# Kernel optimization log

Hardware: AMD Instinct MI355X
Metric: run time of the kernel (lower is better)

The kernel has to match this reference:

```python
import jax, jax.numpy as jnp
import numpy as np

B, L, E, H = 8, 1024, 512, 8
E2 = 2 * E
EPS = 1e-5


def _spectral_fc(x, w, fw, fb, n):
    # rfft along feature dim, multiply by rfft of learned filter w (1,n), irfft back, then Linear
    xf = jnp.fft.rfft(x, axis=2, norm='ortho')          # [B,L,n//2+1] complex
    wf = jnp.fft.rfft(w, axis=1, norm='ortho')          # [1,n//2+1] complex
    y = jnp.fft.irfft(xf * wf, n=n, axis=2, norm='ortho')
    return y @ fw + fb


def _layernorm(x, g, b):
    m = jnp.mean(x, axis=-1, keepdims=True)
    v = jnp.mean(jnp.square(x - m), axis=-1, keepdims=True)
    return (x - m) * jax.lax.rsqrt(v + EPS) * g + b


def setup_inputs() -> dict:
    key = jax.random.key(0)
    ks = jax.random.split(key, 32)
    s = 0.02

    def lin_w(k, i, o):
        return (jax.random.normal(k, (i, o), jnp.float32) / np.sqrt(i)).astype(jnp.float32)

    def layer_params(k0, k1, n):
        return (s * jax.random.normal(k0, (1, n), jnp.float32), lin_w(k1, n, n), jnp.zeros((n,), jnp.float32))

    attn_w, attn_fw, attn_fb = layer_params(ks[1], ks[2], E)
    ln0_w, ln0_fw, ln0_fb = layer_params(ks[3], ks[4], E)
    ln1_w, ln1_fw, ln1_fb = layer_params(ks[5], ks[6], E)
    ln2_w, ln2_fw, ln2_fb = layer_params(ks[7], ks[8], E)
    ln3_w, ln3_fw, ln3_fb = layer_params(ks[9], ks[10], E2)
    ln4_w, ln4_fw, ln4_fb = layer_params(ks[11], ks[12], E2)

    return {
        'x': jax.random.normal(ks[0], (B, L, E), jnp.float32),
        'attn_w': attn_w, 'attn_fw': attn_fw, 'attn_fb': attn_fb,
        'ln0_w': ln0_w, 'ln0_fw': ln0_fw, 'ln0_fb': ln0_fb,
        'ln1_w': ln1_w, 'ln1_fw': ln1_fw, 'ln1_fb': ln1_fb,
        'ln2_w': ln2_w, 'ln2_fw': ln2_fw, 'ln2_fb': ln2_fb,
        'ln3_w': ln3_w, 'ln3_fw': ln3_fw, 'ln3_fb': ln3_fb,
        'ln4_w': ln4_w, 'ln4_fw': ln4_fw, 'ln4_fb': ln4_fb,
        'n1_g': jnp.ones((E,), jnp.float32), 'n1_b': jnp.zeros((E,), jnp.float32),
        'n2_g': jnp.ones((E,), jnp.float32), 'n2_b': jnp.zeros((E,), jnp.float32),
    }


def reference(x, attn_w, attn_fw, attn_fb,
              ln0_w, ln0_fw, ln0_fb, ln1_w, ln1_fw, ln1_fb,
              ln2_w, ln2_fw, ln2_fb, ln3_w, ln3_fw, ln3_fb,
              ln4_w, ln4_fw, ln4_fb, n1_g, n1_b, n2_g, n2_b):
    q = _spectral_fc(x, attn_w, attn_fw, attn_fb, E).reshape(B, L, H, E // H)
    scores = jnp.einsum('blhe,bshe->bhls', q, q) * (1.0 / np.sqrt(E))
    A = jax.nn.softmax(scores, axis=-1)
    new_x = jnp.einsum('bhls,bshd->blhd', A, q).reshape(B, L, E)

    x1 = _layernorm(x + new_x, n1_g, n1_b)
    x_ln = jax.nn.gelu(_spectral_fc(x1, ln0_w, ln0_fw, ln0_fb, E), approximate=False)
    x2 = x1 - x_ln
    h = jax.nn.sigmoid(_spectral_fc(x2, ln1_w, ln1_fw, ln1_fb, E)) * _spectral_fc(x2, ln2_w, ln2_fw, ln2_fb, E)
    out = jnp.concatenate((new_x, x_ln), axis=-1)  # [B,L,2E]
    out = jax.nn.sigmoid(_spectral_fc(out, ln3_w, ln3_fw, ln3_fb, E2)) * _spectral_fc(out, ln4_w, ln4_fw, ln4_fb, E2)
    return (_layernorm(h, n2_g, n2_b), out)
```

## Files before the change

### kernel.cpp

```cpp
#include <hip/hip_runtime.h>
#include <hip/hip_bf16.h>
#include <math.h>

typedef __hip_bfloat16 bf16;
typedef unsigned short u16;
typedef __attribute__((ext_vector_type(8))) short short8;
typedef __attribute__((ext_vector_type(4))) float f32x4;

#define NB      8
#define SEQ     1024
#define EDIM    512
#define E2DIM   1024
#define ROWS    8192
#define INV_SQRT_E 0.04419417382415922f
#define ATT_SCL    0.06375985678148161f

__device__ inline u16 f2bu(float f) {
    union { float f; unsigned u; } c; c.f = f;
    return (u16)((c.u + 0x7FFF + ((c.u >> 16) & 1)) >> 16);
}

__device__ __forceinline__ unsigned cvtpk_bf16(float lo, float hi) {
    unsigned r;
    asm("v_cvt_pk_bf16_f32 %0, %1, %2" : "=v"(r) : "v"(lo), "v"(hi));
    return r;
}

#define VMCNT(N) do { \
    asm volatile("s_waitcnt vmcnt(" #N ")" ::: "memory"); \
    __builtin_amdgcn_sched_barrier(0); \
    __builtin_amdgcn_s_barrier(); \
    __builtin_amdgcn_sched_barrier(0); } while (0)

#define LGKM0_BAR() do { \
    asm volatile("s_waitcnt lgkmcnt(0)" ::: "memory"); \
    __builtin_amdgcn_sched_barrier(0); \
    __builtin_amdgcn_s_barrier(); \
    __builtin_amdgcn_sched_barrier(0); } while (0)

__global__ __launch_bounds__(256) void detect_dtype(const u16* __restrict__ x,
                                                    int* __restrict__ flag) {
    int t = threadIdx.x;
    int cnt = 0;
    for (int k = t; k < 8192; k += 256) {
        int e = (x[k] >> 7) & 0xFF;
        if (e >= 0xC0) cnt++;
    }
#pragma unroll
    for (int o = 32; o > 0; o >>= 1) cnt += __shfl_xor(cnt, o);
    __shared__ int red[4];
    if ((t & 63) == 0) red[t >> 6] = cnt;
    __syncthreads();
    if (t == 0) flag[0] = (red[0] + red[1] + red[2] + red[3] > 100) ? 1 : 0;
}

struct CvtBatch {
    const void* src[23];
    float4*     dst[23];
    int         pre4[24];
};

__global__ __launch_bounds__(256) void cvt_all(CvtBatch a, int total4,
                                               const int* __restrict__ flag) {
    int t = blockIdx.x * 256 + threadIdx.x;
    if (t >= total4) return;
    int lo = 0;
    while (t >= a.pre4[lo + 1]) lo++;
    int li = t - a.pre4[lo];
    if (flag[0]) {
        a.dst[lo][li] = ((const float4*)a.src[lo])[li];
    } else {
        ushort4 u = ((const ushort4*)a.src[lo])[li];
        union { unsigned int i; float f; } c;
        float4 o;
        c.i = ((unsigned)u.x) << 16; o.x = c.f;
        c.i = ((unsigned)u.y) << 16; o.y = c.f;
        c.i = ((unsigned)u.z) << 16; o.z = c.f;
        c.i = ((unsigned)u.w) << 16; o.w = c.f;
        a.dst[lo][li] = o;
    }
}

__global__ __launch_bounds__(256) void f2b_kernel(const float* __restrict__ src,
                                                  u16* __restrict__ dst, int n4) {
    int i = blockIdx.x * 256 + threadIdx.x;
    if (i >= n4) return;
    float4 a = ((const float4*)src)[i];
    ushort4 o;
    o.x = f2bu(a.x); o.y = f2bu(a.y); o.z = f2bu(a.z); o.w = f2bu(a.w);
    ((ushort4*)dst)[i] = o;
}

#define LDK 32

__device__ __forceinline__ void stage128x32(const u16* g, int ld, u16* lds, int tid) {
    const int w = tid >> 6;
    const int l = tid & 63;
    const int r = w * 16 + (l >> 2);
    const int c = ((l & 3) ^ ((l >> 3) & 3)) * 8;
    const u16* g0 = g + (size_t)r * ld + c;
    u16* l0 = lds + w * 16 * LDK;
    __builtin_amdgcn_global_load_lds(
        (const __attribute__((address_space(1))) void*)g0,
        (__attribute__((address_space(3))) void*)l0, 16, 0, 0);
    const u16* g1 = g0 + (size_t)64 * ld;
    u16* l1 = l0 + 64 * LDK;
    __builtin_amdgcn_global_load_lds(
        (const __attribute__((address_space(1))) void*)g1,
        (__attribute__((address_space(3))) void*)l1, 16, 0, 0);
}

__device__ __forceinline__ void stage64x32(const u16* g, int ld, u16* lds, int tid) {
    const int w = tid >> 6;
    const int l = tid & 63;
    const int r = w * 16 + (l >> 2);
    const int c = ((l & 3) ^ ((l >> 3) & 3)) * 8;
    const u16* g0 = g + (size_t)r * ld + c;
    u16* l0 = lds + w * 16 * LDK;
    __builtin_amdgcn_global_load_lds(
        (const __attribute__((address_space(1))) void*)g0,
        (__attribute__((address_space(3))) void*)l0, 16, 0, 0);
}

__device__ __forceinline__ void stage64x64sw(const u16* g0, int ld, u16* lds,
                                             int wave, int lane) {
#pragma unroll
    for (int c = 0; c < 2; c++) {
        const int r  = wave * 16 + c * 8 + (lane >> 3);
        const int cg = (lane & 7) ^ (r & 7);
        const u16* g = g0 + (size_t)r * ld + cg * 8;
        u16* l = lds + (wave * 16 + c * 8) * 64;
        __builtin_amdgcn_global_load_lds(
            (const __attribute__((address_space(1))) void*)g,
            (__attribute__((address_space(3))) void*)l, 16, 0, 0);
    }
}

__device__ __forceinline__ void xcd_swz(int& bx, int& by) {
    const int nx  = gridDim.x;
    const int nwg = nx * gridDim.y;
    const int lid = blockIdx.y * nx + blockIdx.x;
    const int q   = nwg >> 3;
    const int s   = (lid & 7) * q + (lid >> 3);
    bx = s % nx;
    by = s / nx;
}

struct FoldBatch {
    const float* w[6];
    const float* fw[6];
    u16* t1[6];
    u16* t2[6];
    u16* mt[6];
    int  n[6], lg[6];
    float sc[6];
};

__global__ __launch_bounds__(256) void fold_trconv(FoldBatch fb) {
    const int z = blockIdx.z;
    const int n = fb.n[z];
    const int bx = blockIdx.x * 32, by = blockIdx.y * 32;
    if (bx >= n || by >= n) return;
    __shared__ float t[32][33];
    const int tx = threadIdx.x & 31, ty = threadIdx.x >> 5;
    const float* src = fb.fw[z];
    u16* dst = fb.t1[z];
#pragma unroll
    for (int r = 0; r < 32; r += 8)
        t[ty + r][tx] = src[(size_t)(by + ty + r) * n + bx + tx];
    __syncthreads();
#pragma unroll
    for (int r = 0; r < 32; r += 8)
        dst[(size_t)(bx + ty + r) * n + by + tx] = f2bu(t[tx][ty + r]);
}

__global__ __launch_bounds__(256) void fold_circ(FoldBatch fb) {
    const int z = blockIdx.z;
    const int n = fb.n[z], lg = fb.lg[z];
    int idx = blockIdx.x * 256 + threadIdx.x;
    if (idx >= n * n) return;
    int mask = n - 1;
    int m = idx & mask;
    int j = idx >> lg;
    fb.t2[z][idx] = f2bu(fb.w[z][(m - j) & mask]);
}

__global__ __launch_bounds__(256) void fold_gemm(FoldBatch fb) {
    const int z = blockIdx.z;
    const int n = fb.n[z];
    const int bm = blockIdx.y * 128, bn = blockIdx.x * 128;
    if (bm >= n || bn >= n) return;
    const u16* A  = fb.t1[z];
    const u16* Bt = fb.t2[z];
    u16* Mt = fb.mt[z];
    const float scale = fb.sc[z];

    __shared__ u16 Asl[2][128 * LDK];
    __shared__ u16 Bsl[2][128 * LDK];
    const int tid = threadIdx.x;
    const int lane = tid & 63, wave = tid >> 6;
    const int wy = wave >> 1, wx = wave & 1;
    const int qd = lane >> 4, ln16 = lane & 15;
    const int ca = (qd ^ ((ln16 >> 1) & 3)) * 8;

    f32x4 acc[4][4];
#pragma unroll
    for (int i = 0; i < 4; i++)
#pragma unroll
        for (int j = 0; j < 4; j++)
#pragma unroll
            for (int r = 0; r < 4; r++) acc[i][j][r] = 0.f;

    const u16* Ab = A  + (size_t)bm * n;
    const u16* Bb = Bt + (size_t)bn * n;
    const int nt = n >> 5;
    stage128x32(Ab, n, Asl[0], tid);
    stage128x32(Bb, n, Bsl[0], tid);
    stage128x32(Ab + 32, n, Asl[1], tid);
    stage128x32(Bb + 32, n, Bsl[1], tid);
    int cur = 0;
    for (int t = 0; t < nt - 1; ++t) {
        VMCNT(4);
        const u16* Ac = Asl[cur];
        const u16* Bc = Bsl[cur];
        short8 af[4], bf_[4];
#pragma unroll
        for (int i = 0; i < 4; i++) {
            af[i]  = *(const short8*)&Ac[(wy * 64 + i * 16 + ln16) * LDK + ca];
            bf_[i] = *(const short8*)&Bc[(wx * 64 + i * 16 + ln16) * LDK + ca];
        }
        LGKM0_BAR();
        if (t + 2 < nt) {
            const int k2 = (t + 2) * 32;
            stage128x32(Ab + k2, n, Asl[cur], tid);
            stage128x32(Bb + k2, n, Bsl[cur], tid);
        }
#pragma unroll
        for (int i = 0; i < 4; i++)
#pragma unroll
            for (int j = 0; j < 4; j++)
                acc[i][j] = __builtin_amdgcn_mfma_f32_16x16x32_bf16(af[i], bf_[j], acc[i][j], 0, 0, 0);
        cur ^= 1;
    }
    VMCNT(0);
    {
        const u16* Ac = Asl[cur];
        const u16* Bc = Bsl[cur];
        short8 af[4], bf_[4];
#pragma unroll
        for (int i = 0; i < 4; i++) {
            af[i]  = *(const short8*)&Ac[(wy * 64 + i * 16 + ln16) * LDK + ca];
            bf_[i] = *(const short8*)&Bc[(wx * 64 + i * 16 + ln16) * LDK + ca];
        }
#pragma unroll
        for (int i = 0; i < 4; i++)
#pragma unroll
            for (int j = 0; j < 4; j++)
                acc[i][j] = __builtin_amdgcn_mfma_f32_16x16x32_bf16(af[i], bf_[j], acc[i][j], 0, 0, 0);
    }
#pragma unroll
    for (int i = 0; i < 4; i++)
#pragma unroll
        for (int j = 0; j < 4; j++) {
            const int col = bn + wx * 64 + j * 16 + ln16;
#pragma unroll
            for (int r = 0; r < 4; r++) {
                const int row = bm + wy * 64 + i * 16 + qd * 4 + r;
                Mt[(size_t)row * n + col] = f2bu(acc[i][j][r] * scale);
            }
        }
}

__global__ __launch_bounds__(256) void gemm_bf(
    const u16* __restrict__ A, int lda,
    const u16* __restrict__ Bt, int ldb,
    const float* __restrict__ bias,
    float* __restrict__ Cf, int ldc,
    u16* __restrict__ Cb, int ldcb,
    u16* __restrict__ Cb2, int ldcb2,
    const float* __restrict__ aux, int ldaux,
    int K, int mode)
{
    __shared__ u16 Asl[2][128 * LDK];
    __shared__ u16 Bsl[2][64 * LDK];
    const int tid = threadIdx.x;
    int bxs, bys;
    xcd_swz(bxs, bys);
    const int bm = bys * 128, bn = bxs * 64;
    const int lane = tid & 63, wave = tid >> 6;
    const int wy = wave >> 1, wx = wave & 1;
    const int qd = lane >> 4, ln16 = lane & 15;
    const int ca = (qd ^ ((ln16 >> 1) & 3)) * 8;

    f32x4 acc[4][2];
#pragma unroll
    for (int i = 0; i < 4; i++)
#pragma unroll
        for (int j = 0; j < 2; j++)
#pragma unroll
            for (int r = 0; r < 4; r++) acc[i][j][r] = 0.f;

    const u16* Ab = A  + (size_t)bm * lda;
    const u16* Bb = Bt + (size_t)bn * ldb;
    const int nt = K >> 5;
    stage128x32(Ab, lda, Asl[0], tid);
    stage64x32(Bb, ldb, Bsl[0], tid);
    stage128x32(Ab + 32, lda, Asl[1], tid);
    stage64x32(Bb + 32, ldb, Bsl[1], tid);
    int cur = 0;
    for (int t = 0; t < nt - 1; ++t) {
        VMCNT(3);
        const u16* Ac = Asl[cur];
        const u16* Bc = Bsl[cur];
        short8 af[4], bf_[2];
#pragma unroll
        for (int i = 0; i < 4; i++)
            af[i]  = *(const short8*)&Ac[(wy * 64 + i * 16 + ln16) * LDK + ca];
#pragma unroll
        for (int j = 0; j < 2; j++)
            bf_[j] = *(const short8*)&Bc[(wx * 32 + j * 16 + ln16) * LDK + ca];
        LGKM0_BAR();
        if (t + 2 < nt) {
            const int k2 = (t + 2) * 32;
            stage128x32(Ab + k2, lda, Asl[cur], tid);
            stage64x32(Bb + k2, ldb, Bsl[cur], tid);
        }
#pragma unroll
        for (int i = 0; i < 4; i++)
#pragma unroll
            for (int j = 0; j < 2; j++)
                acc[i][j] = __builtin_amdgcn_mfma_f32_16x16x32_bf16(af[i], bf_[j], acc[i][j], 0, 0, 0);
        cur ^= 1;
    }
    VMCNT(0);
    {
        const u16* Ac = Asl[cur];
        const u16* Bc = Bsl[cur];
        short8 af[4], bf_[2];
#pragma unroll
        for (int i = 0; i < 4; i++)
            af[i]  = *(const short8*)&Ac[(wy * 64 + i * 16 + ln16) * LDK + ca];
#pragma unroll
        for (int j = 0; j < 2; j++)
            bf_[j] = *(const short8*)&Bc[(wx * 32 + j * 16 + ln16) * LDK + ca];
#pragma unroll
        for (int i = 0; i < 4; i++)
#pragma unroll
            for (int j = 0; j < 2; j++)
                acc[i][j] = __builtin_amdgcn_mfma_f32_16x16x32_bf16(af[i], bf_[j], acc[i][j], 0, 0, 0);
    }

#pragma unroll
    for (int i = 0; i < 4; i++) {
#pragma unroll
        for (int j = 0; j < 2; j++) {
            const int col = bn + wx * 32 + j * 16 + ln16;
            const float b_ = bias ? bias[col] : 0.f;
#pragma unroll
            for (int r = 0; r < 4; r++) {
                const int row = bm + wy * 64 + i * 16 + qd * 4 + r;
                float v = acc[i][j][r] + b_;
                if (mode == 1) v = 0.5f * v * (1.0f + erff(v * 0.7071067811865476f));
                if (Cf)  Cf[(size_t)row * ldc + col] = v;
                if (Cb)  Cb[(size_t)row * ldcb + col] = f2bu(v);
                if (Cb2) Cb2[(size_t)row * ldcb2 + col] =
                             f2bu(aux[(size_t)row * ldaux + col] - v);
            }
        }
    }
}

__global__ __launch_bounds__(256) void gemm_bf2(
    const u16* __restrict__ A, int lda,
    const u16* __restrict__ B1t, const u16* __restrict__ B2t, int ldb,
    const float* __restrict__ bias1, const float* __restrict__ bias2,
    float* __restrict__ Cf, int ldc, int K)
{
    __shared__ u16 Asl[2][128 * LDK];
    __shared__ u16 B1sl[2][64 * LDK];
    __shared__ u16 B2sl[2][64 * LDK];
    const int tid = threadIdx.x;
    int bxs, bys;
    xcd_swz(bxs, bys);
    const int bm = bys * 128, bn = bxs * 64;
    const int lane = tid & 63, wave = tid >> 6;
    const int wy = wave >> 1, wx = wave & 1;
    const int qd = lane >> 4, ln16 = lane & 15;
    const int ca = (qd ^ ((ln16 >> 1) & 3)) * 8;

    f32x4 acc1[4][2], acc2[4][2];
#pragma unroll
    for (int i = 0; i < 4; i++)
#pragma unroll
        for (int j = 0; j < 2; j++)
#pragma unroll
            for (int r = 0; r < 4; r++) { acc1[i][j][r] = 0.f; acc2[i][j][r] = 0.f; }

    const u16* Ab  = A   + (size_t)bm * lda;
    const u16* B1b = B1t + (size_t)bn * ldb;
    const u16* B2b = B2t + (size_t)bn * ldb;
    const int nt = K >> 5;
    stage128x32(Ab,  lda, Asl[0],  tid);
    stage64x32(B1b, ldb, B1sl[0], tid);
    stage64x32(B2b, ldb, B2sl[0], tid);
    stage128x32(Ab + 32,  lda, Asl[1],  tid);
    stage64x32(B1b + 32, ldb, B1sl[1], tid);
    stage64x32(B2b + 32, ldb, B2sl[1], tid);
    int cur = 0;
    for (int t = 0; t < nt - 1; ++t) {
        VMCNT(4);
        const u16* Ac  = Asl[cur];
        const u16* B1c = B1sl[cur];
        const u16* B2c = B2sl[cur];
        short8 af[4], b1f[2], b2f[2];
#pragma unroll
        for (int i = 0; i < 4; i++)
            af[i]  = *(const short8*)&Ac [(wy * 64 + i * 16 + ln16) * LDK + ca];
#pragma unroll
        for (int j = 0; j < 2; j++) {
            b1f[j] = *(const short8*)&B1c[(wx * 32 + j * 16 + ln16) * LDK + ca];
            b2f[j] = *(const short8*)&B2c[(wx * 32 + j * 16 + ln16) * LDK + ca];
        }
        LGKM0_BAR();
        if (t + 2 < nt) {
            const int k2 = (t + 2) * 32;
            stage128x32(Ab  + k2, lda, Asl[cur],  tid);
            stage64x32(B1b + k2, ldb, B1sl[cur], tid);
            stage64x32(B2b + k2, ldb, B2sl[cur], tid);
        }
#pragma unroll
        for (int i = 0; i < 4; i++)
#pragma unroll
            for (int j = 0; j < 2; j++) {
                acc1[i][j] = __builtin_amdgcn_mfma_f32_16x16x32_bf16(af[i], b1f[j], acc1[i][j], 0, 0, 0);
                acc2[i][j] = __builtin_amdgcn_mfma_f32_16x16x32_bf16(af[i], b2f[j], acc2[i][j], 0, 0, 0);
            }
        cur ^= 1;
    }
    VMCNT(0);
    {
        const u16* Ac  = Asl[cur];
        const u16* B1c = B1sl[cur];
        const u16* B2c = B2sl[cur];
        short8 af[4], b1f[2], b2f[2];
#pragma unroll
        for (int i = 0; i < 4; i++)
            af[i]  = *(const short8*)&Ac [(wy * 64 + i * 16 + ln16) * LDK + ca];
#pragma unroll
        for (int j = 0; j < 2; j++) {
            b1f[j] = *(const short8*)&B1c[(wx * 32 + j * 16 + ln16) * LDK + ca];
            b2f[j] = *(const short8*)&B2c[(wx * 32 + j * 16 + ln16) * LDK + ca];
        }
#pragma unroll
        for (int i = 0; i < 4; i++)
#pragma unroll
            for (int j = 0; j < 2; j++) {
                acc1[i][j] = __builtin_amdgcn_mfma_f32_16x16x32_bf16(af[i], b1f[j], acc1[i][j], 0, 0, 0);
                acc2[i][j] = __builtin_amdgcn_mfma_f32_16x16x32_bf16(af[i], b2f[j], acc2[i][j], 0, 0, 0);
            }
    }

#pragma unroll
    for (int i = 0; i < 4; i++) {
#pragma unroll
        for (int j = 0; j < 2; j++) {
            const int col = bn + wx * 32 + j * 16 + ln16;
            const float b1_ = bias1[col], b2_ = bias2[col];
#pragma unroll
            for (int r = 0; r < 4; r++) {
                const int row = bm + wy * 64 + i * 16 + qd * 4 + r;
                const float g = 1.0f / (1.0f + expf(-(acc1[i][j][r] + b1_)));
                Cf[(size_t)row * ldc + col] = g * (acc2[i][j][r] + b2_);
            }
        }
    }
}

__global__ __launch_bounds__(256) void ln_kernel(
    const float* __restrict__ in0, int ld0,
    const u16* __restrict__ in1b, int ld1b,
    const float* __restrict__ g, const float* __restrict__ bta,
    float* __restrict__ outf, int ldo,
    u16* __restrict__ outb, int ldob)
{
    int row = blockIdx.x, tid = threadIdx.x;
    const float* p0 = in0 + (size_t)row * ld0;
    float v0 = p0[tid], v1 = p0[tid + 256];
    if (in1b) {
        const u16* p1 = in1b + (size_t)row * ld1b;
        union { unsigned u; float f; } c0, c1;
        c0.u = ((unsigned)p1[tid]) << 16;
        c1.u = ((unsigned)p1[tid + 256]) << 16;
        v0 += c0.f; v1 += c1.f;
    }
    float s = v0 + v1, sq = v0 * v0 + v1 * v1;
#pragma unroll
    for (int o = 32; o > 0; o >>= 1) {
        s  += __shfl_xor(s, o);
        sq += __shfl_xor(sq, o);
    }
    __shared__ float red[8];
    int wid = tid >> 6;
    if ((tid & 63) == 0) { red[wid] = s; red[4 + wid] = sq; }
    __syncthreads();
    s  = red[0] + red[1] + red[2] + red[3];
    sq = red[4] + red[5] + red[6] + red[7];
    float mean = s * (1.0f / 512.0f);
    float var  = sq * (1.0f / 512.0f) - mean * mean;
    float rstd = rsqrtf(var + 1e-5f);
    float o0 = (v0 - mean) * rstd * g[tid] + bta[tid];
    float o1 = (v1 - mean) * rstd * g[tid + 256] + bta[tid + 256];
    if (outf) {
        outf[(size_t)row * ldo + tid]       = o0;
        outf[(size_t)row * ldo + tid + 256] = o1;
    }
    if (outb) {
        outb[(size_t)row * ldob + tid]       = f2bu(o0);
        outb[(size_t)row * ldob + tid + 256] = f2bu(o1);
    }
}

__global__ __launch_bounds__(256) void trans_vt(const u16* __restrict__ q,
                                                u16* __restrict__ vt) {
    const int z  = blockIdx.z;
    const int bb = z >> 3, hh = z & 7;
    const int k0 = blockIdx.x * 64;
    const int d0 = blockIdx.y * 32;
    __shared__ u16 t[64][33];
    const int tx = threadIdx.x & 31, ty = threadIdx.x >> 5;
    const u16* src = q + (size_t)(bb * SEQ + k0) * EDIM + hh * 64 + d0;
#pragma unroll
    for (int r = 0; r < 64; r += 8)
        t[ty + r][tx] = src[(size_t)(ty + r) * EDIM + tx];
    __syncthreads();
    const int ox = threadIdx.x & 63, oy = threadIdx.x >> 6;
    u16* dst = vt + ((size_t)z * 64 + d0) * SEQ + k0;
#pragma unroll
    for (int r = 0; r < 32; r += 4)
        dst[(size_t)(oy + r) * SEQ + ox] = t[ox][oy + r];
}

#define AP 80
#define ANT 16

__global__ __launch_bounds__(256) void attn_mfma(const u16* __restrict__ qall,
                                                 const u16* __restrict__ vt,
                                                 u16* __restrict__ catb) {
    __shared__ u16 Ks[64 * 64];
    __shared__ u16 VTs[64 * 64];
    __shared__ u16 Pw[4][16 * AP];

    const int phys = blockIdx.x;
    const int bid = (phys & 7) * 128 + (phys >> 3);
    const int lt = bid & 15, hh = (bid >> 4) & 7, bb = bid >> 7;
    const int q0 = lt * 64;
    const int tid = threadIdx.x;
    const int wave = tid >> 6, lane = tid & 63;
    const int quad = lane >> 4, ln16 = lane & 15;

    const u16* qh = qall + (size_t)bb * SEQ * EDIM + hh * 64;
    const u16* vh = vt + (size_t)(bb * 8 + hh) * 64 * SEQ;

    const u16* qrow = qh + (size_t)(q0 + wave * 16 + ln16) * EDIM + quad * 8;
    const short8 aq0 = *(const short8*)(qrow);
    const short8 aq1 = *(const short8*)(qrow + 32);

    f32x4 oacc[4];
    float m_run = -1e30f, l_run = 0.f;
#pragma unroll
    for (int j = 0; j < 4; j++)
#pragma unroll
        for (int r = 0; r < 4; r++) oacc[j][r] = 0.f;

    const int sw = ln16 & 7;
    const int c0 = (quad ^ sw) * 8;
    const int c1 = ((quad + 4) ^ sw) * 8;

    for (int t = 0; t < ANT; ++t) {
        if (t) __syncthreads();
        stage64x64sw(qh + (size_t)t * 64 * EDIM, EDIM, Ks, wave, lane);
        stage64x64sw(vh + t * 64, SEQ, VTs, wave, lane);
        __syncthreads();

        f32x4 S[4];
#pragma unroll
        for (int j = 0; j < 4; j++) {
            const int ro = (j * 16 + ln16) * 64;
            short8 a0 = *(const short8*)&Ks[ro + c0];
            short8 a1 = *(const short8*)&Ks[ro + c1];
            f32x4 c = {0.f, 0.f, 0.f, 0.f};
            c = __builtin_amdgcn_mfma_f32_16x16x32_bf16(a0, aq0, c, 0, 0, 0);
            c = __builtin_amdgcn_mfma_f32_16x16x32_bf16(a1, aq1, c, 0, 0, 0);
            S[j] = c;
        }

        float mx = S[0][0];
#pragma unroll
        for (int j = 0; j < 4; j++)
#pragma unroll
            for (int r = 0; r < 4; r++) mx = fmaxf(mx, S[j][r]);
        mx = fmaxf(mx, __shfl_xor(mx, 16));
        mx = fmaxf(mx, __shfl_xor(mx, 32));
        const float mn = fmaxf(m_run, mx);
        const float al = exp2f((m_run - mn) * ATT_SCL);
        m_run = mn;
        const float ns = -mn * ATT_SCL;
        float p[4][4];
        float rs = 0.f;
#pragma unroll
        for (int j = 0; j < 4; j++)
#pragma unroll
            for (int r = 0; r < 4; r++) {
                p[j][r] = exp2f(fmaf(S[j][r], ATT_SCL, ns));
                rs += p[j][r];
            }
        rs += __shfl_xor(rs, 16);
        rs += __shfl_xor(rs, 32);
        l_run = l_run * al + rs;

#pragma unroll
        for (int j = 0; j < 4; j++) {
            unsigned w0 = cvtpk_bf16(p[j][0], p[j][1]);
            unsigned w1 = cvtpk_bf16(p[j][2], p[j][3]);
            *(uint2*)&Pw[wave][ln16 * AP + j * 16 + quad * 4] = make_uint2(w0, w1);
        }

        float alq[4];
#pragma unroll
        for (int r = 0; r < 4; r++) alq[r] = __shfl(al, quad * 4 + r);
#pragma unroll
        for (int j = 0; j < 4; j++)
#pragma unroll
            for (int r = 0; r < 4; r++) oacc[j][r] *= alq[r];

        short8 pa0 = *(const short8*)&Pw[wave][ln16 * AP + quad * 8];
        short8 pa1 = *(const short8*)&Pw[wave][ln16 * AP + 32 + quad * 8];
#pragma unroll
        for (int j = 0; j < 4; j++) {
            const int ro = (j * 16 + ln16) * 64;
            short8 b0 = *(const short8*)&VTs[ro + c0];
            short8 b1 = *(const short8*)&VTs[ro + c1];
            oacc[j] = __builtin_amdgcn_mfma_f32_16x16x32_bf16(pa0, b0, oacc[j], 0, 0, 0);
            oacc[j] = __builtin_amdgcn_mfma_f32_16x16x32_bf16(pa1, b1, oacc[j], 0, 0, 0);
        }
    }

    const float linv = 1.0f / l_run;
    float invq[4];
#pragma unroll
    for (int r = 0; r < 4; r++) invq[r] = __shfl(linv, quad * 4 + r);
#pragma unroll
    for (int r = 0; r < 4; r++) {
        const int row = bb * SEQ + q0 + wave * 16 + quad * 4 + r;
#pragma unroll
        for (int j = 0; j < 4; j++) {
            const int col = hh * 64 + j * 16 + ln16;
            catb[(size_t)row * E2DIM + col] = f2bu(oacc[j][r] * invq[r]);
        }
    }
}

extern "C" void kernel_launch(void* const* d_in, const int* in_sizes, int n_in,
                              void* d_out, int out_size, void* d_ws, size_t ws_size,
                              hipStream_t stream)
{
    const size_t OFF_MT0 = 0;
    const size_t OFF_MT1 = OFF_MT0 + 131072;
    const size_t OFF_MT2 = OFF_MT1 + 131072;
    const size_t OFF_MT3 = OFF_MT2 + 131072;
    const size_t OFF_MT4 = OFF_MT3 + 131072;
    const size_t OFF_MT5 = OFF_MT4 + 524288;
    const size_t OFF_XB  = OFF_MT5 + 524288;
    const size_t OFF_CB  = OFF_XB + 2097152;
    const size_t OFF_BQ  = OFF_CB + 4194304;
    const size_t OFF_BN  = OFF_BQ + 4194304;
    const size_t OFF_BC  = OFF_BN + 4194304;
    const size_t OFF_P   = OFF_BC + 4194304;

    float* W = (float*)d_ws;
    u16* MT[6] = {(u16*)(W + OFF_MT0), (u16*)(W + OFF_MT1), (u16*)(W + OFF_MT2),
                  (u16*)(W + OFF_MT3), (u16*)(W + OFF_MT4), (u16*)(W + OFF_MT5)};
    u16*   XB  = (u16*)(W + OFF_XB);
    u16*   CB  = (u16*)(W + OFF_CB);
    u16*   QB  = (u16*)(W + OFF_BQ);
    float* BN  = W + OFF_BN;
    float* BC  = W + OFF_BC;
    u16*   VT  = (u16*)BN;

    float* F[23];
    CvtBatch cb;
    int pre = 0;
    for (int i = 0; i < 23 && i < n_in; i++) {
        cb.pre4[i] = pre;
        F[i] = W + OFF_P + (size_t)pre * 4;
        cb.src[i] = d_in[i];
        cb.dst[i] = (float4*)F[i];
        pre += in_sizes[i] / 4;
    }
    cb.pre4[23] = pre;
    const int total4 = pre;
    int* FLAG = (int*)(W + OFF_P + (size_t)total4 * 4);

    if (n_in < 23) return;
    if (ws_size < (OFF_P + (size_t)total4 * 4 + 16) * sizeof(float)) return;

    detect_dtype<<<1, 256, 0, stream>>>((const u16*)d_in[0], FLAG);
    cvt_all<<<(total4 + 255) / 256, 256, 0, stream>>>(cb, total4, FLAG);
    f2b_kernel<<<(ROWS * EDIM / 4 + 255) / 256, 256, 0, stream>>>(F[0], XB, ROWS * EDIM / 4);

    FoldBatch fb;
    {
        const int wi[6] = {1, 4, 7, 10, 13, 16};
        u16* T1 = (u16*)BN;
        u16* T2 = (u16*)BC;
        size_t off = 0;
        for (int s = 0; s < 6; s++) {
            const int n = (s < 4) ? 512 : 1024;
            fb.w[s]  = F[wi[s]];
            fb.fw[s] = F[wi[s] + 1];
            fb.t1[s] = T1 + off;
            fb.t2[s] = T2 + off;
            fb.mt[s] = MT[s];
            fb.n[s]  = n;
            fb.lg[s] = (s < 4) ? 9 : 10;
            fb.sc[s] = (s < 4) ? 0.04419417382415922f : 0.03125f;
            off += (size_t)n * n;
        }
    }
    fold_trconv<<<dim3(32, 32, 6), 256, 0, stream>>>(fb);
    fold_circ<<<dim3(4096, 1, 6), 256, 0, stream>>>(fb);
    fold_gemm<<<dim3(8, 8, 6), 256, 0, stream>>>(fb);

    float* out0 = (float*)d_out;
    float* out1 = (float*)d_out + (size_t)ROWS * EDIM;

    gemm_bf<<<dim3(8, 64), 256, 0, stream>>>(
        XB, 512, MT[0], 512, F[3], nullptr, 0, QB, 512, nullptr, 0, nullptr, 0, 512, 0);
    trans_vt<<<dim3(16, 2, 64), 256, 0, stream>>>(QB, VT);
    attn_mfma<<<1024, 256, 0, stream>>>(QB, VT, CB);
    ln_kernel<<<8192, 256, 0, stream>>>(F[0], 512, CB, 1024, F[19], F[20],
                                        BC, 512, XB, 512);
    gemm_bf<<<dim3(8, 64), 256, 0, stream>>>(
        XB, 512, MT[1], 512, F[6], nullptr, 0, CB + 512, 1024, QB, 512, BC, 512, 512, 1);
    gemm_bf2<<<dim3(8, 64), 256, 0, stream>>>(
        QB, 512, MT[2], MT[3], 512, F[9], F[12], BN, 512, 512);
    ln_kernel<<<8192, 256, 0, stream>>>(BN, 512, nullptr, 0, F[21], F[22],
                                        out0, 512, nullptr, 0);
    gemm_bf2<<<dim3(16, 64), 256, 0, stream>>>(
        CB, 1024, MT[4], MT[5], 1024, F[15], F[18], out1, 1024, 1024);
}
```

Baseline: 333.6 us.

## Triple-buffer GEMM LDS staging and drop the second barrier per k-step

Moves the three GEMM kernels from double-buffered to triple-buffered LDS tiles. Prefetches then write into a buffer that is not being read, so the lgkmcnt wait and second workgroup barrier before each prefetch can be removed. Staging addresses are also precomputed once and advanced by pointer increments, and the peeled final iteration is folded into the loop. This costs more LDS per block, which may lower occupancy, and correctness now depends on the single vmcnt barrier being enough to order reads and overwrites across three buffers.

```diff
diff --git a/kernel.cpp b/kernel.cpp
--- a/kernel.cpp
+++ b/kernel.cpp
@@ -32,11 +32,11 @@
     __builtin_amdgcn_s_barrier(); \
     __builtin_amdgcn_sched_barrier(0); } while (0)
 
-#define LGKM0_BAR() do { \
-    asm volatile("s_waitcnt lgkmcnt(0)" ::: "memory"); \
-    __builtin_amdgcn_sched_barrier(0); \
-    __builtin_amdgcn_s_barrier(); \
-    __builtin_amdgcn_sched_barrier(0); } while (0)
+__device__ __forceinline__ void dma16(const u16* g, u16* l) {
+    __builtin_amdgcn_global_load_lds(
+        (const __attribute__((address_space(1))) void*)g,
+        (__attribute__((address_space(3))) void*)l, 16, 0, 0);
+}
 
 __global__ __launch_bounds__(256) void detect_dtype(const u16* __restrict__ x,
                                                     int* __restrict__ flag) {
@@ -93,35 +93,6 @@
 
 #define LDK 32
 
-__device__ __forceinline__ void stage128x32(const u16* g, int ld, u16* lds, int tid) {
-    const int w = tid >> 6;
-    const int l = tid & 63;
-    const int r = w * 16 + (l >> 2);
-    const int c = ((l & 3) ^ ((l >> 3) & 3)) * 8;
-    const u16* g0 = g + (size_t)r * ld + c;
-    u16* l0 = lds + w * 16 * LDK;
-    __builtin_amdgcn_global_load_lds(
-        (const __attribute__((address_space(1))) void*)g0,
-        (__attribute__((address_space(3))) void*)l0, 16, 0, 0);
-    const u16* g1 = g0 + (size_t)64 * ld;
-    u16* l1 = l0 + 64 * LDK;
-    __builtin_amdgcn_global_load_lds(
-        (const __attribute__((address_space(1))) void*)g1,
-        (__attribute__((address_space(3))) void*)l1, 16, 0, 0);
-}
-
-__device__ __forceinline__ void stage64x32(const u16* g, int ld, u16* lds, int tid) {
-    const int w = tid >> 6;
-    const int l = tid & 63;
-    const int r = w * 16 + (l >> 2);
-    const int c = ((l & 3) ^ ((l >> 3) & 3)) * 8;
-    const u16* g0 = g + (size_t)r * ld + c;
-    u16* l0 = lds + w * 16 * LDK;
-    __builtin_amdgcn_global_load_lds(
-        (const __attribute__((address_space(1))) void*)g0,
-        (__attribute__((address_space(3))) void*)l0, 16, 0, 0);
-}
-
 __device__ __forceinline__ void stage64x64sw(const u16* g0, int ld, u16* lds,
                                              int wave, int lane) {
 #pragma unroll
@@ -130,9 +101,7 @@
         const int cg = (lane & 7) ^ (r & 7);
         const u16* g = g0 + (size_t)r * ld + cg * 8;
         u16* l = lds + (wave * 16 + c * 8) * 64;
-        __builtin_amdgcn_global_load_lds(
-            (const __attribute__((address_space(1))) void*)g,
-            (__attribute__((address_space(3))) void*)l, 16, 0, 0);
+        dma16(g, l);
     }
 }
 
@@ -195,14 +164,21 @@
     u16* Mt = fb.mt[z];
     const float scale = fb.sc[z];
 
-    __shared__ u16 Asl[2][128 * LDK];
-    __shared__ u16 Bsl[2][128 * LDK];
+    __shared__ u16 Asl[3][128 * LDK];
+    __shared__ u16 Bsl[3][128 * LDK];
     const int tid = threadIdx.x;
     const int lane = tid & 63, wave = tid >> 6;
     const int wy = wave >> 1, wx = wave & 1;
     const int qd = lane >> 4, ln16 = lane & 15;
     const int ca = (qd ^ ((ln16 >> 1) & 3)) * 8;
 
+    const int srow = wave * 16 + (lane >> 2);
+    const int scol = ((lane & 3) ^ ((lane >> 3) & 3)) * 8;
+    const int lo   = wave * 16 * LDK;
+    const size_t a64 = (size_t)64 * n;
+    const u16* pA = A  + (size_t)bm * n + (size_t)srow * n + scol;
+    const u16* pB = Bt + (size_t)bn * n + (size_t)srow * n + scol;
+
     f32x4 acc[4][4];
 #pragma unroll
     for (int i = 0; i < 4; i++)
@@ -211,16 +187,19 @@
 #pragma unroll
             for (int r = 0; r < 4; r++) acc[i][j][r] = 0.f;
 
-    const u16* Ab = A  + (size_t)bm * n;
-    const u16* Bb = Bt + (size_t)bn * n;
+#define STAGE_FG(bi) do { \
+    dma16(pA,       &Asl[bi][lo]); \
+    dma16(pA + a64, &Asl[bi][lo + 64 * LDK]); \
+    dma16(pB,       &Bsl[bi][lo]); \
+    dma16(pB + a64, &Bsl[bi][lo + 64 * LDK]); \
+    pA += 32; pB += 32; } while (0)
+
     const int nt = n >> 5;
-    stage128x32(Ab, n, Asl[0], tid);
-    stage128x32(Bb, n, Bsl[0], tid);
-    stage128x32(Ab + 32, n, Asl[1], tid);
-    stage128x32(Bb + 32, n, Bsl[1], tid);
-    int cur = 0;
-    for (int t = 0; t < nt - 1; ++t) {
-        VMCNT(4);
+    STAGE_FG(0);
+    STAGE_FG(1);
+    int cur = 0, stg = 2;
+    for (int t = 0; t < nt; ++t) {
+        if (t < nt - 1) { VMCNT(4); } else { VMCNT(0); }
         const u16* Ac = Asl[cur];
         const u16* Bc = Bsl[cur];
         short8 af[4], bf_[4];
@@ -229,35 +208,16 @@
             af[i]  = *(const short8*)&Ac[(wy * 64 + i * 16 + ln16) * LDK + ca];
             bf_[i] = *(const short8*)&Bc[(wx * 64 + i * 16 + ln16) * LDK + ca];
         }
-        LGKM0_BAR();
-        if (t + 2 < nt) {
-            const int k2 = (t + 2) * 32;
-            stage128x32(Ab + k2, n, Asl[cur], tid);
-            stage128x32(Bb + k2, n, Bsl[cur], tid);
-        }
+        if (t + 2 < nt) STAGE_FG(stg);
 #pragma unroll
         for (int i = 0; i < 4; i++)
 #pragma unroll
             for (int j = 0; j < 4; j++)
                 acc[i][j] = __builtin_amdgcn_mfma_f32_16x16x32_bf16(af[i], bf_[j], acc[i][j], 0, 0, 0);
-        cur ^= 1;
-    }
-    VMCNT(0);
-    {
-        const u16* Ac = Asl[cur];
-        const u16* Bc = Bsl[cur];
-        short8 af[4], bf_[4];
-#pragma unroll
-        for (int i = 0; i < 4; i++) {
-            af[i]  = *(const short8*)&Ac[(wy * 64 + i * 16 + ln16) * LDK + ca];
-            bf_[i] = *(const short8*)&Bc[(wx * 64 + i * 16 + ln16) * LDK + ca];
-        }
-#pragma unroll
-        for (int i = 0; i < 4; i++)
-#pragma unroll
-            for (int j = 0; j < 4; j++)
-                acc[i][j] = __builtin_amdgcn_mfma_f32_16x16x32_bf16(af[i], bf_[j], acc[i][j], 0, 0, 0);
-    }
+        cur = (cur == 2) ? 0 : cur + 1;
+        stg = (stg == 2) ? 0 : stg + 1;
+    }
+#undef STAGE_FG
 #pragma unroll
     for (int i = 0; i < 4; i++)
 #pragma unroll
@@ -281,8 +241,8 @@
     const float* __restrict__ aux, int ldaux,
     int K, int mode)
 {
-    __shared__ u16 Asl[2][128 * LDK];
-    __shared__ u16 Bsl[2][64 * LDK];
+    __shared__ u16 Asl[3][128 * LDK];
+    __shared__ u16 Bsl[3][64 * LDK];
     const int tid = threadIdx.x;
     int bxs, bys;
     xcd_swz(bxs, bys);
@@ -292,6 +252,13 @@
     const int qd = lane >> 4, ln16 = lane & 15;
     const int ca = (qd ^ ((ln16 >> 1) & 3)) * 8;
 
+    const int srow = wave * 16 + (lane >> 2);
+    const int scol = ((lane & 3) ^ ((lane >> 3) & 3)) * 8;
+    const int lo   = wave * 16 * LDK;
+    const size_t a64 = (size_t)64 * lda;
+    const u16* pA = A  + (size_t)bm * lda + (size_t)srow * lda + scol;
+    const u16* pB = Bt + (size_t)bn * ldb + (size_t)srow * ldb + scol;
+
     f32x4 acc[4][2];
 #pragma unroll
     for (int i = 0; i < 4; i++)
@@ -300,16 +267,18 @@
 #pragma unroll
             for (int r = 0; r < 4; r++) acc[i][j][r] = 0.f;
 
-    const u16* Ab = A  + (size_t)bm * lda;
-    const u16* Bb = Bt + (size_t)bn * ldb;
+#define STAGE_GB(bi) do { \
+    dma16(pA,       &Asl[bi][lo]); \
+    dma16(pA + a64, &Asl[bi][lo + 64 * LDK]); \
+    dma16(pB,       &Bsl[bi][lo]); \
+    pA += 32; pB += 32; } while (0)
+
     const int nt = K >> 5;
-    stage128x32(Ab, lda, Asl[0], tid);
-    stage64x32(Bb, ldb, Bsl[0], tid);
-    stage128x32(Ab + 32, lda, Asl[1], tid);
-    stage64x32(Bb + 32, ldb, Bsl[1], tid);
-    int cur = 0;
-    for (int t = 0; t < nt - 1; ++t) {
-        VMCNT(3);
+    STAGE_GB(0);
+    STAGE_GB(1);
+    int cur = 0, stg = 2;
+    for (int t = 0; t < nt; ++t) {
+        if (t < nt - 1) { VMCNT(3); } else { VMCNT(0); }
         const u16* Ac = Asl[cur];
         const u16* Bc = Bsl[cur];
         short8 af[4], bf_[2];
@@ -319,36 +288,16 @@
 #pragma unroll
         for (int j = 0; j < 2; j++)
             bf_[j] = *(const short8*)&Bc[(wx * 32 + j * 16 + ln16) * LDK + ca];
-        LGKM0_BAR();
-        if (t + 2 < nt) {
-            const int k2 = (t + 2) * 32;
-            stage128x32(Ab + k2, lda, Asl[cur], tid);
-            stage64x32(Bb + k2, ldb, Bsl[cur], tid);
-        }
+        if (t + 2 < nt) STAGE_GB(stg);
 #pragma unroll
         for (int i = 0; i < 4; i++)
 #pragma unroll
             for (int j = 0; j < 2; j++)
                 acc[i][j] = __builtin_amdgcn_mfma_f32_16x16x32_bf16(af[i], bf_[j], acc[i][j], 0, 0, 0);
-        cur ^= 1;
-    }
-    VMCNT(0);
-    {
-        const u16* Ac = Asl[cur];
-        const u16* Bc = Bsl[cur];
-        short8 af[4], bf_[2];
-#pragma unroll
-        for (int i = 0; i < 4; i++)
-            af[i]  = *(const short8*)&Ac[(wy * 64 + i * 16 + ln16) * LDK + ca];
-#pragma unroll
-        for (int j = 0; j < 2; j++)
-            bf_[j] = *(const short8*)&Bc[(wx * 32 + j * 16 + ln16) * LDK + ca];
-#pragma unroll
-        for (int i = 0; i < 4; i++)
-#pragma unroll
-            for (int j = 0; j < 2; j++)
-                acc[i][j] = __builtin_amdgcn_mfma_f32_16x16x32_bf16(af[i], bf_[j], acc[i][j], 0, 0, 0);
-    }
+        cur = (cur == 2) ? 0 : cur + 1;
+        stg = (stg == 2) ? 0 : stg + 1;
+    }
+#undef STAGE_GB
 
 #pragma unroll
     for (int i = 0; i < 4; i++) {
@@ -376,9 +325,9 @@
     const float* __restrict__ bias1, const float* __restrict__ bias2,
     float* __restrict__ Cf, int ldc, int K)
 {
-    __shared__ u16 Asl[2][128 * LDK];
-    __shared__ u16 B1sl[2][64 * LDK];
-    __shared__ u16 B2sl[2][64 * LDK];
+    __shared__ u16 Asl[3][128 * LDK];
+    __shared__ u16 B1sl[3][64 * LDK];
+    __shared__ u16 B2sl[3][64 * LDK];
     const int tid = threadIdx.x;
     int bxs, bys;
     xcd_swz(bxs, bys);
@@ -388,6 +337,14 @@
     const int qd = lane >> 4, ln16 = lane & 15;
     const int ca = (qd ^ ((ln16 >> 1) & 3)) * 8;
 
+    const int srow = wave * 16 + (lane >> 2);
+    const int scol = ((lane & 3) ^ ((lane >> 3) & 3)) * 8;
+    const int lo   = wave * 16 * LDK;
+    const size_t a64 = (size_t)64 * lda;
+    const u16* pA  = A   + (size_t)bm * lda + (size_t)srow * lda + scol;
+    const u16* pB1 = B1t + (size_t)bn * ldb + (size_t)srow * ldb + scol;
+    const u16* pB2 = B2t + (size_t)bn * ldb + (size_t)srow * ldb + scol;
+
     f32x4 acc1[4][2], acc2[4][2];
 #pragma unroll
     for (int i = 0; i < 4; i++)
@@ -396,19 +353,19 @@
 #pragma unroll
             for (int r = 0; r < 4; r++) { acc1[i][j][r] = 0.f; acc2[i][j][r] = 0.f; }
 
-    const u16* Ab  = A   + (size_t)bm * lda;
-    const u16* B1b = B1t + (size_t)bn * ldb;
-    const u16* B2b = B2t + (size_t)bn * ldb;
+#define STAGE_GB2(bi) do { \
+    dma16(pA,       &Asl[bi][lo]); \
+    dma16(pA + a64, &Asl[bi][lo + 64 * LDK]); \
+    dma16(pB1,      &B1sl[bi][lo]); \
+    dma16(pB2,      &B2sl[bi][lo]); \
+    pA += 32; pB1 += 32; pB2 += 32; } while (0)
+
     const int nt = K >> 5;
-    stage128x32(Ab,  lda, Asl[0],  tid);
-    stage64x32(B1b, ldb, B1sl[0], tid);
-    stage64x32(B2b, ldb, B2sl[0], tid);
-    stage128x32(Ab + 32,  lda, Asl[1],  tid);
-    stage64x32(B1b + 32, ldb, B1sl[1], tid);
-    stage64x32(B2b + 32, ldb, B2sl[1], tid);
-    int cur = 0;
-    for (int t = 0; t < nt - 1; ++t) {
-        VMCNT(4);
+    STAGE_GB2(0);
+    STAGE_GB2(1);
+    int cur = 0, stg = 2;
+    for (int t = 0; t < nt; ++t) {
+        if (t < nt - 1) { VMCNT(4); } else { VMCNT(0); }
         const u16* Ac  = Asl[cur];
         const u16* B1c = B1sl[cur];
         const u16* B2c = B2sl[cur];
@@ -421,13 +378,7 @@
             b1f[j] = *(const short8*)&B1c[(wx * 32 + j * 16 + ln16) * LDK + ca];
             b2f[j] = *(const short8*)&B2c[(wx * 32 + j * 16 + ln16) * LDK + ca];
         }
-        LGKM0_BAR();
-        if (t + 2 < nt) {
-            const int k2 = (t + 2) * 32;
-            stage128x32(Ab  + k2, lda, Asl[cur],  tid);
-            stage64x32(B1b + k2, ldb, B1sl[cur], tid);
-            stage64x32(B2b + k2, ldb, B2sl[cur], tid);
-        }
+        if (t + 2 < nt) STAGE_GB2(stg);
 #pragma unroll
         for (int i = 0; i < 4; i++)
 #pragma unroll
@@ -435,30 +386,10 @@
                 acc1[i][j] = __builtin_amdgcn_mfma_f32_16x16x32_bf16(af[i], b1f[j], acc1[i][j], 0, 0, 0);
                 acc2[i][j] = __builtin_amdgcn_mfma_f32_16x16x32_bf16(af[i], b2f[j], acc2[i][j], 0, 0, 0);
             }
-        cur ^= 1;
-    }
-    VMCNT(0);
-    {
-        const u16* Ac  = Asl[cur];
-        const u16* B1c = B1sl[cur];
-        const u16* B2c = B2sl[cur];
-        short8 af[4], b1f[2], b2f[2];
-#pragma unroll
-        for (int i = 0; i < 4; i++)
-            af[i]  = *(const short8*)&Ac [(wy * 64 + i * 16 + ln16) * LDK + ca];
-#pragma unroll
-        for (int j = 0; j < 2; j++) {
-            b1f[j] = *(const short8*)&B1c[(wx * 32 + j * 16 + ln16) * LDK + ca];
-            b2f[j] = *(const short8*)&B2c[(wx * 32 + j * 16 + ln16) * LDK + ca];
-        }
-#pragma unroll
-        for (int i = 0; i < 4; i++)
-#pragma unroll
-            for (int j = 0; j < 2; j++) {
-                acc1[i][j] = __builtin_amdgcn_mfma_f32_16x16x32_bf16(af[i], b1f[j], acc1[i][j], 0, 0, 0);
-                acc2[i][j] = __builtin_amdgcn_mfma_f32_16x16x32_bf16(af[i], b2f[j], acc2[i][j], 0, 0, 0);
-            }
-    }
+        cur = (cur == 2) ? 0 : cur + 1;
+        stg = (stg == 2) ? 0 : stg + 1;
+    }
+#undef STAGE_GB2
 
 #pragma unroll
     for (int i = 0; i < 4; i++) {
```

Result: no change. 331.4 us (-0.7%).
